# Performance work log

Measured on AMD Instinct MI355X. Metric: run time of the kernel, lower is better.

The kernel has to match this reference:

```python
import jax, jax.numpy as jnp
import numpy as np

NUM_USERS = 100000
NUM_ITEMS = 50000
N_NODES = NUM_USERS + NUM_ITEMS
N_INTERACTIONS = 1000000
LATENT_DIM = 32
K = 4
N_LAYERS = 3
BATCH = 4096


def setup_inputs() -> dict:
    key = jax.random.key(0)
    k_u, k_i = jax.random.split(key)
    # torch init: normal std=0.1
    user_emb = 0.1 * jax.random.normal(k_u, (NUM_USERS, LATENT_DIM * K), dtype=jnp.float32)
    item_emb = 0.1 * jax.random.normal(k_i, (NUM_ITEMS, LATENT_DIM * K), dtype=jnp.float32)
    # build symmetric normalized bipartite adjacency (LightGCN getSparseGraph)
    rng = np.random.default_rng(0)
    u = rng.integers(0, NUM_USERS, N_INTERACTIONS)
    it = rng.integers(0, NUM_ITEMS, N_INTERACTIONS)
    src = np.concatenate([u, it + NUM_USERS]).astype(np.int32)
    dst = np.concatenate([it + NUM_USERS, u]).astype(np.int32)
    deg = np.bincount(src, minlength=N_NODES).astype(np.float32)
    deg = np.maximum(deg, 1.0)
    val = (1.0 / np.sqrt(deg[src] * deg[dst])).astype(np.float32)
    users = rng.integers(0, NUM_USERS, BATCH).astype(np.int32)
    items = rng.integers(0, NUM_ITEMS, BATCH).astype(np.int32)
    return {
        "user_emb": user_emb,
        "item_emb": item_emb,
        "edge_src": jnp.asarray(src),
        "edge_dst": jnp.asarray(dst),
        "edge_val": jnp.asarray(val),
        "users": jnp.asarray(users),
        "items": jnp.asarray(items),
    }


def _computer(user_emb, item_emb, edge_src, edge_dst, edge_val):
    n_users = user_emb.shape[0]
    n = n_users + item_emb.shape[0]
    # [N, K, D] disentangled factor view of the K*D embedding
    x = jnp.concatenate([user_emb, item_emb], axis=0).reshape(n, K, -1)
    embs = [x]
    for _ in range(N_LAYERS):
        # SpMM over all K factor slices at once: out[dst] += val * x[src]
        msgs = x[edge_src] * edge_val[:, None, None]  # [E, K, D]
        x = jax.ops.segment_sum(msgs, edge_dst, num_segments=n)
        embs.append(x)
    light_out = jnp.mean(jnp.stack(embs, axis=1), axis=1)  # [N, K, D]
    return light_out[:n_users], light_out[n_users:]


def reference(user_emb, item_emb, edge_src, edge_dst, edge_val, users, items):
    all_users, all_items = _computer(user_emb, item_emb, edge_src, edge_dst, edge_val)
    u = all_users[users]   # [B, K, D]
    i = all_items[items]   # [B, K, D]
    return jnp.sum(u * i, axis=(-1, -2))  # [B]
```

## Files before the change

### kernel.cpp

```cpp
#include <hip/hip_runtime.h>

#define NUM_USERS 100000
#define NUM_ITEMS 50000
#define N_NODES   150000
#define N_EDGES   2000000
#define DIM       128
#define DIM4      32
#define CH8       16
#define BATCH     4096
#define B_SHIFT   9
#define BUCK_N    (1 << B_SHIFT)
#define NBUCK     ((N_NODES + BUCK_N - 1) >> B_SHIFT)
#define CHUNK     8192
#define NCHUNK    ((N_EDGES + CHUNK - 1) / CHUNK)
#define CAP       12288
#define CAPB      16384
#define MARK_BLOCKS 512
#define CONV_BLOCKS ((N_NODES * CH8 + 255) / 256)

typedef _Float16 half_t;
typedef __attribute__((ext_vector_type(8))) _Float16 half8;


__global__ void bucket_scatter_kernel(const int* __restrict__ src,
                                      const int* __restrict__ dst,
                                      int* __restrict__ bcur,
                                      int* __restrict__ tmp) {
    __shared__ int lhist[NBUCK];
    __shared__ int lcur[NBUCK];
    int t = threadIdx.x;
    int base = blockIdx.x * CHUNK;
    for (int i = t; i < NBUCK; i += 512) lhist[i] = 0;
    __syncthreads();
    for (int i = 0; i < CHUNK / 512; ++i) {
        int e = base + i * 512 + t;
        if (e < N_EDGES) atomicAdd(&lhist[dst[e] >> B_SHIFT], 1);
    }
    __syncthreads();
    for (int i = t; i < NBUCK; i += 512) {
        int c = lhist[i];
        lcur[i] = c ? (i * CAPB + atomicAdd(&bcur[i], c)) : 0;
    }
    __syncthreads();
    for (int i = 0; i < CHUNK / 512; ++i) {
        int e = base + i * 512 + t;
        if (e < N_EDGES) {
            int d = dst[e];
            int buck = d >> B_SHIFT;
            int pos = atomicAdd(&lcur[buck], 1);
            if (pos < (buck + 1) * CAPB)
                tmp[pos] = (src[e] << B_SHIFT) | (d & (BUCK_N - 1));
        }
    }
}


__global__ void place_kernel(const int* __restrict__ bcur,
                             const int* __restrict__ tmp,
                             int* __restrict__ row_start,
                             float* __restrict__ rinv,
                             float* __restrict__ sdeg,
                             int* __restrict__ csr_src) {
    __shared__ int lhist[BUCK_N];
    __shared__ int lofs[BUCK_N];
    __shared__ int ssc[512];
    __shared__ int outbuf[CAP];
    int b = blockIdx.x;
    int t = threadIdx.x;

    int c = 0;
    if (t < NBUCK) {
        c = bcur[t];
        if (c > CAPB) c = CAPB;
    }
    ssc[t] = c;
    __syncthreads();
    for (int off = 1; off < 512; off <<= 1) {
        int v = (t >= off) ? ssc[t - off] : 0;
        __syncthreads();
        ssc[t] += v;
        __syncthreads();
    }
    int beg = (b == 0) ? 0 : ssc[b - 1];
    int end = ssc[b];
    int cnt = end - beg;
    int tbase = b * CAPB;
    int n0 = b << B_SHIFT;
    int n1 = n0 + BUCK_N; if (n1 > N_NODES) n1 = N_NODES;
    if (b == NBUCK - 1 && t == 0) row_start[N_NODES] = end;

    lhist[t] = 0;
    __syncthreads();
    for (int e = t; e < cnt; e += 512)
        atomicAdd(&lhist[tmp[tbase + e] & (BUCK_N - 1)], 1);
    __syncthreads();

    int v = lhist[t];
    ssc[t] = v;
    __syncthreads();
    for (int off = 1; off < 512; off <<= 1) {
        int u = (t >= off) ? ssc[t - off] : 0;
        __syncthreads();
        ssc[t] += u;
        __syncthreads();
    }
    int excl = ssc[t] - v;
    lofs[t] = excl;
    int node = n0 + t;
    if (node < n1) {
        row_start[node] = beg + excl;
        float d = (float)(v > 1 ? v : 1);
        float rr = rsqrtf(d);
        rinv[node] = rr;
        sdeg[node] = d * rr;
    }
    __syncthreads();

    if (cnt <= CAP) {
        for (int e = t; e < cnt; e += 512) {
            int p = tmp[tbase + e];
            int pos = atomicAdd(&lofs[p & (BUCK_N - 1)], 1);
            outbuf[pos] = p >> B_SHIFT;
        }
        __syncthreads();
        for (int i = t; i < cnt; i += 512) csr_src[beg + i] = outbuf[i];
    } else {
        for (int e = t; e < cnt; e += 512) {
            int p = tmp[tbase + e];
            int pos = atomicAdd(&lofs[p & (BUCK_N - 1)], 1);
            csr_src[beg + pos] = p >> B_SHIFT;
        }
    }
}


__global__ void mark_conv_kernel(const float4* __restrict__ ue4,
                                 const float4* __restrict__ ie4,
                                 const float* __restrict__ rinv,
                                 half8* __restrict__ e16,
                                 const int* __restrict__ users,
                                 const int* __restrict__ items,
                                 const int* __restrict__ row_start,
                                 const int* __restrict__ csr_src,
                                 int* __restrict__ mark) {
    int bid = blockIdx.x;
    if (bid < MARK_BLOCKS) {
        int g = threadIdx.x >> 4;
        int lane = threadIdx.x & 15;
        int b = bid * 16 + g;
        int node = (b < BATCH) ? users[b] : (NUM_USERS + items[b - BATCH]);
        if (lane == 0) mark[node] = 1;
        int beg = row_start[node], end = row_start[node + 1];
        for (int e = beg + lane; e < end; e += 16) mark[csr_src[e]] = 1;
        return;
    }
    int i = (bid - MARK_BLOCKS) * 256 + threadIdx.x;
    const int total = N_NODES * CH8;
    if (i >= total) return;
    int n = i >> 4;
    int j = i & 15;
    const float4* row = (n < NUM_USERS) ? ue4 + (size_t)n * DIM4
                                        : ie4 + (size_t)(n - NUM_USERS) * DIM4;
    float r = rinv[n];
    float4 f0 = row[2 * j];
    float4 f1 = row[2 * j + 1];
    half8 h;
    h[0] = (half_t)(r * f0.x); h[1] = (half_t)(r * f0.y);
    h[2] = (half_t)(r * f0.z); h[3] = (half_t)(r * f0.w);
    h[4] = (half_t)(r * f1.x); h[5] = (half_t)(r * f1.y);
    h[6] = (half_t)(r * f1.z); h[7] = (half_t)(r * f1.w);
    e16[i] = h;
}


__global__ void spmm16_kernel(const half8* __restrict__ in16,
                              const int* __restrict__ row_start,
                              const int* __restrict__ csr_src,
                              const float* __restrict__ rinv,
                              half8* __restrict__ out16) {
    int g = threadIdx.x >> 4;
    int lane = threadIdx.x & 15;
    int n = blockIdx.x * 16 + g;
    if (n >= N_NODES) return;
    int beg = row_start[n], end = row_start[n + 1];
    float a[8];
#pragma unroll
    for (int j = 0; j < 8; ++j) a[j] = 0.f;
    int e = beg;
    for (; e + 4 <= end; e += 4) {
        int s0 = csr_src[e], s1 = csr_src[e + 1], s2 = csr_src[e + 2], s3 = csr_src[e + 3];
        half8 h0 = in16[(size_t)s0 * CH8 + lane];
        half8 h1 = in16[(size_t)s1 * CH8 + lane];
        half8 h2 = in16[(size_t)s2 * CH8 + lane];
        half8 h3 = in16[(size_t)s3 * CH8 + lane];
#pragma unroll
        for (int j = 0; j < 8; ++j)
            a[j] += ((float)h0[j] + (float)h1[j]) + ((float)h2[j] + (float)h3[j]);
    }
    for (; e < end; ++e) {
        int s0 = csr_src[e];
        half8 h0 = in16[(size_t)s0 * CH8 + lane];
#pragma unroll
        for (int j = 0; j < 8; ++j) a[j] += (float)h0[j];
    }
    float f = rinv[n]; f *= f;
    half8 o;
#pragma unroll
    for (int j = 0; j < 8; ++j) o[j] = (half_t)(a[j] * f);
    out16[(size_t)n * CH8 + lane] = o;
}


__global__ void spmm16_masked_kernel(const half8* __restrict__ in16,
                                     const int* __restrict__ row_start,
                                     const int* __restrict__ csr_src,
                                     const float* __restrict__ rinv,
                                     const int* __restrict__ mark,
                                     half8* __restrict__ out16) {
    int g = threadIdx.x >> 4;
    int lane = threadIdx.x & 15;
    int n = blockIdx.x * 16 + g;
    if (n >= N_NODES) return;
    if (!mark[n]) return;
    int beg = row_start[n], end = row_start[n + 1];
    float a[8];
#pragma unroll
    for (int j = 0; j < 8; ++j) a[j] = 0.f;
    int e = beg;
    for (; e + 4 <= end; e += 4) {
        int s0 = csr_src[e], s1 = csr_src[e + 1], s2 = csr_src[e + 2], s3 = csr_src[e + 3];
        half8 h0 = in16[(size_t)s0 * CH8 + lane];
        half8 h1 = in16[(size_t)s1 * CH8 + lane];
        half8 h2 = in16[(size_t)s2 * CH8 + lane];
        half8 h3 = in16[(size_t)s3 * CH8 + lane];
#pragma unroll
        for (int j = 0; j < 8; ++j)
            a[j] += ((float)h0[j] + (float)h1[j]) + ((float)h2[j] + (float)h3[j]);
    }
    for (; e < end; ++e) {
        int s0 = csr_src[e];
        half8 h0 = in16[(size_t)s0 * CH8 + lane];
#pragma unroll
        for (int j = 0; j < 8; ++j) a[j] += (float)h0[j];
    }
    float f = rinv[n]; f *= f;
    half8 o;
#pragma unroll
    for (int j = 0; j < 8; ++j) o[j] = (half_t)(a[j] * f);
    out16[(size_t)n * CH8 + lane] = o;
}


__global__ void epilogue_kernel(const float4* __restrict__ ue4,
                                const float4* __restrict__ ie4,
                                const half8* __restrict__ w1,
                                const half8* __restrict__ w2,
                                const int* __restrict__ row_start,
                                const int* __restrict__ csr_src,
                                const float* __restrict__ rinv,
                                const float* __restrict__ sdeg,
                                const int* __restrict__ users,
                                const int* __restrict__ items,
                                float* __restrict__ out) {
    int t = threadIdx.x;
    int elem = blockIdx.x * 4 + (t >> 5);
    int half = (t >> 4) & 1;
    int lane = t & 15;
    int node = half ? (NUM_USERS + items[elem]) : users[elem];

    const float4* erow = (node < NUM_USERS) ? ue4 + (size_t)node * DIM4
                                            : ie4 + (size_t)(node - NUM_USERS) * DIM4;
    float4 f0 = erow[2 * lane];
    float4 f1 = erow[2 * lane + 1];
    float a[8] = {f0.x, f0.y, f0.z, f0.w, f1.x, f1.y, f1.z, f1.w};

    float sd = sdeg[node];
    half8 h1 = w1[(size_t)node * CH8 + lane];
    half8 h2 = w2[(size_t)node * CH8 + lane];
#pragma unroll
    for (int j = 0; j < 8; ++j) a[j] += sd * ((float)h1[j] + (float)h2[j]);

    int beg = row_start[node], end = row_start[node + 1];
    float a3[8];
#pragma unroll
    for (int j = 0; j < 8; ++j) a3[j] = 0.f;
    int e = beg;
    for (; e + 2 <= end; e += 2) {
        int s0 = csr_src[e], s1 = csr_src[e + 1];
        half8 g0 = w2[(size_t)s0 * CH8 + lane];
        half8 g1 = w2[(size_t)s1 * CH8 + lane];
#pragma unroll
        for (int j = 0; j < 8; ++j) a3[j] += (float)g0[j] + (float)g1[j];
    }
    if (e < end) {
        int s0 = csr_src[e];
        half8 g0 = w2[(size_t)s0 * CH8 + lane];
#pragma unroll
        for (int j = 0; j < 8; ++j) a3[j] += (float)g0[j];
    }
    float rv = rinv[node];
#pragma unroll
    for (int j = 0; j < 8; ++j) a[j] += rv * a3[j];

    int wl = t & 63;
    float p = 0.f;
#pragma unroll
    for (int j = 0; j < 8; ++j) p += a[j] * __shfl(a[j], wl ^ 16, 64);
    for (int off = 8; off > 0; off >>= 1) p += __shfl_down(p, off, 16);
    if (half == 0 && lane == 0) out[elem] = p * (1.0f / 16.0f);
}

extern "C" void kernel_launch(void* const* d_in, const int* in_sizes, int n_in,
                              void* d_out, int out_size, void* d_ws, size_t ws_size,
                              hipStream_t stream) {
    const float4* ue4 = (const float4*)d_in[0];
    const float4* ie4 = (const float4*)d_in[1];
    const int*   src   = (const int*)d_in[2];
    const int*   dst   = (const int*)d_in[3];
    const int*   users = (const int*)d_in[5];
    const int*   items = (const int*)d_in[6];
    float* out = (float*)d_out;

    const size_t h8elems = (size_t)N_NODES * CH8;
    char* ws = (char*)d_ws;
    half8* e16       = (half8*)ws;  ws += h8elems * sizeof(half8);
    half8* w1        = (half8*)ws;  ws += h8elems * sizeof(half8);
    half8* w2        = (half8*)ws;  ws += h8elems * sizeof(half8);
    int*   row_start = (int*)ws;    ws += (size_t)(N_NODES + 1) * sizeof(int);
    float* rinv      = (float*)ws;  ws += (size_t)N_NODES * sizeof(float);
    float* sdeg      = (float*)ws;  ws += (size_t)N_NODES * sizeof(float);
    int*   mark      = (int*)ws;    ws += (size_t)N_NODES * sizeof(int);
    int*   bcur      = (int*)ws;    ws += (size_t)NBUCK * sizeof(int);
    ws = (char*)(((size_t)ws + 255) & ~(size_t)255);
    int*   tmp       = (int*)ws;    ws += (size_t)NBUCK * CAPB * sizeof(int);
    int*   csr_src   = (int*)ws;    ws += (size_t)N_EDGES * sizeof(int);

    hipMemsetAsync(mark, 0, (size_t)N_NODES * sizeof(int) + (size_t)NBUCK * sizeof(int), stream);

    bucket_scatter_kernel<<<NCHUNK, 512, 0, stream>>>(src, dst, bcur, tmp);
    place_kernel<<<NBUCK, 512, 0, stream>>>(bcur, tmp, row_start, rinv, sdeg, csr_src);

    mark_conv_kernel<<<MARK_BLOCKS + CONV_BLOCKS, 256, 0, stream>>>(
        ue4, ie4, rinv, e16, users, items, row_start, csr_src, mark);

    spmm16_kernel<<<(N_NODES + 15) / 16, 256, 0, stream>>>(e16, row_start, csr_src, rinv, w1);

    spmm16_masked_kernel<<<(N_NODES + 15) / 16, 256, 0, stream>>>(
        w1, row_start, csr_src, rinv, mark, w2);

    epilogue_kernel<<<BATCH / 4, 128, 0, stream>>>(
        ue4, ie4, w1, w2, row_start, csr_src, rinv, sdeg, users, items, out);
}
```

Baseline: 305.6 us.

## Assign one wavefront per node in SpMM with cooperative edge loads and shuffles

Replaces the 16-thread-per-node SpMM kernels with a templated kernel that gives each node a full 64-lane wavefront. Each lane loads one edge index, and the indices are broadcast with shuffles so four 16-lane quarters gather different neighbour rows in parallel. The partial sums are then reduced across quarters with xor-shuffles. This aims to raise memory-level parallelism and coalesce index loads, at the cost of idle lanes on low-degree nodes, shuffle overhead, and four times as many blocks.

```diff
diff --git a/kernel.cpp b/kernel.cpp
--- a/kernel.cpp
+++ b/kernel.cpp
@@ -173,81 +173,72 @@
 }
 
 
-__global__ void spmm16_kernel(const half8* __restrict__ in16,
-                              const int* __restrict__ row_start,
-                              const int* __restrict__ csr_src,
-                              const float* __restrict__ rinv,
-                              half8* __restrict__ out16) {
-    int g = threadIdx.x >> 4;
-    int lane = threadIdx.x & 15;
-    int n = blockIdx.x * 16 + g;
+template <int MASKED>
+__global__ __launch_bounds__(256) void spmm_wave_kernel(
+        const half8* __restrict__ in16,
+        const int* __restrict__ row_start,
+        const int* __restrict__ csr_src,
+        const float* __restrict__ rinv,
+        const int* __restrict__ mark,
+        half8* __restrict__ out16) {
+    int n = blockIdx.x * 4 + (threadIdx.x >> 6);
     if (n >= N_NODES) return;
+    if (MASKED && !mark[n]) return;
+    int lane = threadIdx.x & 63;
+    int q = lane >> 4;
+    int c = lane & 15;
     int beg = row_start[n], end = row_start[n + 1];
     float a[8];
 #pragma unroll
     for (int j = 0; j < 8; ++j) a[j] = 0.f;
-    int e = beg;
-    for (; e + 4 <= end; e += 4) {
-        int s0 = csr_src[e], s1 = csr_src[e + 1], s2 = csr_src[e + 2], s3 = csr_src[e + 3];
-        half8 h0 = in16[(size_t)s0 * CH8 + lane];
-        half8 h1 = in16[(size_t)s1 * CH8 + lane];
-        half8 h2 = in16[(size_t)s2 * CH8 + lane];
-        half8 h3 = in16[(size_t)s3 * CH8 + lane];
-#pragma unroll
-        for (int j = 0; j < 8; ++j)
-            a[j] += ((float)h0[j] + (float)h1[j]) + ((float)h2[j] + (float)h3[j]);
-    }
-    for (; e < end; ++e) {
-        int s0 = csr_src[e];
-        half8 h0 = in16[(size_t)s0 * CH8 + lane];
-#pragma unroll
-        for (int j = 0; j < 8; ++j) a[j] += (float)h0[j];
-    }
-    float f = rinv[n]; f *= f;
-    half8 o;
-#pragma unroll
-    for (int j = 0; j < 8; ++j) o[j] = (half_t)(a[j] * f);
-    out16[(size_t)n * CH8 + lane] = o;
-}
-
-
-__global__ void spmm16_masked_kernel(const half8* __restrict__ in16,
-                                     const int* __restrict__ row_start,
-                                     const int* __restrict__ csr_src,
-                                     const float* __restrict__ rinv,
-                                     const int* __restrict__ mark,
-                                     half8* __restrict__ out16) {
-    int g = threadIdx.x >> 4;
-    int lane = threadIdx.x & 15;
-    int n = blockIdx.x * 16 + g;
-    if (n >= N_NODES) return;
-    if (!mark[n]) return;
-    int beg = row_start[n], end = row_start[n + 1];
-    float a[8];
-#pragma unroll
-    for (int j = 0; j < 8; ++j) a[j] = 0.f;
-    int e = beg;
-    for (; e + 4 <= end; e += 4) {
-        int s0 = csr_src[e], s1 = csr_src[e + 1], s2 = csr_src[e + 2], s3 = csr_src[e + 3];
-        half8 h0 = in16[(size_t)s0 * CH8 + lane];
-        half8 h1 = in16[(size_t)s1 * CH8 + lane];
-        half8 h2 = in16[(size_t)s2 * CH8 + lane];
-        half8 h3 = in16[(size_t)s3 * CH8 + lane];
-#pragma unroll
-        for (int j = 0; j < 8; ++j)
-            a[j] += ((float)h0[j] + (float)h1[j]) + ((float)h2[j] + (float)h3[j]);
-    }
-    for (; e < end; ++e) {
-        int s0 = csr_src[e];
-        half8 h0 = in16[(size_t)s0 * CH8 + lane];
-#pragma unroll
-        for (int j = 0; j < 8; ++j) a[j] += (float)h0[j];
-    }
-    float f = rinv[n]; f *= f;
-    half8 o;
-#pragma unroll
-    for (int j = 0; j < 8; ++j) o[j] = (half_t)(a[j] * f);
-    out16[(size_t)n * CH8 + lane] = o;
+
+    for (int base = beg; base < end; base += 64) {
+        int eidx = base + lane;
+        int myedge = (eidx < end) ? csr_src[eidx] : 0;
+        int m = end - base; if (m > 64) m = 64;
+        int nblk = (m + 15) >> 4;
+        for (int blk = 0; blk < nblk; ++blk) {
+            int sl = 16 * blk + q;
+            int s0 = __shfl(myedge, sl,      64);
+            int s1 = __shfl(myedge, sl + 4,  64);
+            int s2 = __shfl(myedge, sl + 8,  64);
+            int s3 = __shfl(myedge, sl + 12, 64);
+            half8 h0 = in16[(s0 << 4) + c];
+            half8 h1 = in16[(s1 << 4) + c];
+            half8 h2 = in16[(s2 << 4) + c];
+            half8 h3 = in16[(s3 << 4) + c];
+            int e0 = base + sl;
+            if (e0 < end) {
+#pragma unroll
+                for (int j = 0; j < 8; ++j) a[j] += (float)h0[j];
+            }
+            if (e0 + 4 < end) {
+#pragma unroll
+                for (int j = 0; j < 8; ++j) a[j] += (float)h1[j];
+            }
+            if (e0 + 8 < end) {
+#pragma unroll
+                for (int j = 0; j < 8; ++j) a[j] += (float)h2[j];
+            }
+            if (e0 + 12 < end) {
+#pragma unroll
+                for (int j = 0; j < 8; ++j) a[j] += (float)h3[j];
+            }
+        }
+    }
+
+#pragma unroll
+    for (int j = 0; j < 8; ++j) {
+        a[j] += __shfl_xor(a[j], 16, 64);
+        a[j] += __shfl_xor(a[j], 32, 64);
+    }
+    if (q == 0) {
+        float f = rinv[n]; f *= f;
+        half8 o;
+#pragma unroll
+        for (int j = 0; j < 8; ++j) o[j] = (half_t)(a[j] * f);
+        out16[((size_t)n << 4) + c] = o;
+    }
 }
 
 
@@ -343,9 +334,10 @@
     mark_conv_kernel<<<MARK_BLOCKS + CONV_BLOCKS, 256, 0, stream>>>(
         ue4, ie4, rinv, e16, users, items, row_start, csr_src, mark);
 
-    spmm16_kernel<<<(N_NODES + 15) / 16, 256, 0, stream>>>(e16, row_start, csr_src, rinv, w1);
-
-    spmm16_masked_kernel<<<(N_NODES + 15) / 16, 256, 0, stream>>>(
+    spmm_wave_kernel<0><<<(N_NODES + 3) / 4, 256, 0, stream>>>(
+        e16, row_start, csr_src, rinv, nullptr, w1);
+
+    spmm_wave_kernel<1><<<(N_NODES + 3) / 4, 256, 0, stream>>>(
         w1, row_start, csr_src, rinv, mark, w2);
 
     epilogue_kernel<<<BATCH / 4, 128, 0, stream>>>(
```

Measured after the change: 313.5 us. +2.6%, slower.
